# Performance work log

Measured on AMD Instinct MI355X. Metric: run time of the kernel, lower is better.

## Reference

```python
import jax, jax.numpy as jnp
import numpy as np

N_NODES = 100000


def _gcn_conv(x, W, b, src, dst, n):
    # PyG GCNConv (default): add self-loops, norm = deg^{-1/2}[src] * deg^{-1/2}[dst]
    # degree computed on target nodes (col) with unit edge weights, then
    # out[i] = sum_{(j->i)} norm_ji * (x_j @ W) + b
    loops = jnp.arange(n, dtype=src.dtype)
    s = jnp.concatenate([src, loops])
    d = jnp.concatenate([dst, loops])
    deg = jax.ops.segment_sum(jnp.ones_like(d, dtype=x.dtype), d, num_segments=n)
    dinv = jnp.where(deg > 0, jax.lax.rsqrt(deg), 0.0)
    h = x @ W                                  # [n, out_dim]
    norm = (dinv[s] * dinv[d])[:, None]        # [E+n, 1]
    msg = h[s] * norm                          # gather + scale
    out = jax.ops.segment_sum(msg, d, num_segments=n)  # scatter-add to targets
    return out + b


def setup_inputs() -> dict:
    key = jax.random.key(0)
    ks = jax.random.split(key, 4)
    x = jax.random.normal(ks[0], (N_NODES, 128), dtype=jnp.float32)
    edge_index = jax.random.randint(ks[1], (2, 1600000), 0, N_NODES, dtype=jnp.int64)
    W1 = jax.random.normal(ks[2], (128, 16), dtype=jnp.float32) * (1.0 / np.sqrt(128))
    b1 = jnp.zeros((16,), dtype=jnp.float32)
    W2 = jax.random.normal(ks[3], (16, 3), dtype=jnp.float32) * (1.0 / np.sqrt(16))
    b2 = jnp.zeros((3,), dtype=jnp.float32)
    return {"x": x, "edge_index": edge_index, "W1": W1, "b1": b1, "W2": W2, "b2": b2}


def reference(x, edge_index, W1, b1, W2, b2):
    src, dst = edge_index[0], edge_index[1]
    n = x.shape[0]
    h = _gcn_conv(x, W1, b1, src, dst, n)
    h = jax.nn.relu(h)
    # F.dropout in eval mode == identity (deterministic baseline)
    h = _gcn_conv(h, W2, b2, src, dst, n)
    return jax.nn.log_softmax(h, axis=1)
```

## Files before the change

### kernel.cpp

```cpp
#include <hip/hip_runtime.h>
#include <hip/hip_fp16.h>
#include <math.h>


#define BSH 9
#define BNODES 512
#define P1 512
#define GROWS 64
#define K2BUF 10240
#define BCAP 12288
#define EPT 16

struct alignas(8) Half4 { __half x, y, z, w; };

__global__ void k1a_count(const int* __restrict__ dst, int* __restrict__ hist_t,
                          int NBK, int E) {
    __shared__ int lh[256];
    int t = threadIdx.x;
    lh[t] = 0;
    __syncthreads();
    int slice = (E + P1 - 1) / P1;
    int e0 = blockIdx.x * slice, e1 = min(E, e0 + slice);
    for (int e = e0 + t; e < e1; e += 256)
        atomicAdd(&lh[dst[e] >> BSH], 1);
    __syncthreads();
    for (int i = t; i < NBK; i += 256)
        hist_t[(size_t)i * P1 + blockIdx.x] = lh[i];
}

__global__ void kscan1(const int* __restrict__ hist_t, int* __restrict__ colpre_t,
                       int* __restrict__ btot, int NBK) {
    __shared__ int v[P1], part[256];
    int kb = blockIdx.x, t = threadIdx.x;
    v[t] = hist_t[(size_t)kb * P1 + t];
    v[t + 256] = hist_t[(size_t)kb * P1 + t + 256];
    __syncthreads();
    int a = v[2 * t], c = v[2 * t + 1];
    part[t] = a + c;
    __syncthreads();
    for (int o = 1; o < 256; o <<= 1) {
        int add = (t >= o) ? part[t - o] : 0;
        __syncthreads();
        part[t] += add;
        __syncthreads();
    }
    int pre = (t == 0) ? 0 : part[t - 1];
    colpre_t[(size_t)kb * P1 + 2 * t] = pre;
    colpre_t[(size_t)kb * P1 + 2 * t + 1] = pre + a;
    if (t == 255) btot[kb] = part[255];
}

__global__ void k1b_fat(const int* __restrict__ src, const int* __restrict__ dst,
                        const int* __restrict__ colpre_t,
                        unsigned int* __restrict__ staging,
                        const float* __restrict__ x, const float* __restrict__ W1,
                        Half4* __restrict__ g1h, int NBK, int n, int E) {
    __shared__ float sx[GROWS * 132];
    __shared__ float4 sW4[512];
    int b = blockIdx.x;
    if (b < P1) {
        int* hist  = (int*)sx;
        int* cs    = hist + 256;
        int* loff  = hist + 512;
        int* cur   = hist + 768;
        int* buf   = hist + 1024;
        int* gaddr = buf + 3200;
        int t = threadIdx.x;
        hist[t] = 0; cur[t] = 0;
        for (int i = t; i < NBK; i += 256)
            loff[i] = i * BCAP + colpre_t[(size_t)i * P1 + b];
        __syncthreads();
        int slice = (E + P1 - 1) / P1;
        int e0 = b * slice, e1 = min(E, e0 + slice);
        int len = e1 - e0;
        int dl[EPT], sl[EPT];
        int cnt = 0;
        for (int e = e0 + t; e < e1 && cnt < EPT; e += 256, ++cnt) {
            dl[cnt] = dst[e];
            sl[cnt] = src[e];
        }
        for (int i = 0; i < cnt; ++i)
            atomicAdd(&hist[dl[i] >> BSH], 1);
        __syncthreads();
        int h = hist[t];
        cs[t] = h;
        __syncthreads();
        for (int o = 1; o < 256; o <<= 1) {
            int add = (t >= o) ? cs[t - o] : 0;
            __syncthreads();
            cs[t] += add;
            __syncthreads();
        }
        int incl = cs[t];
        __syncthreads();
        cs[t] = incl - h;
        __syncthreads();
        for (int i = 0; i < cnt; ++i) {
            int d = dl[i], s = sl[i];
            int k = d >> BSH;
            int tk = atomicAdd(&cur[k], 1);
            int pos = cs[k] + tk;
            buf[pos] = (s << BSH) | (d & (BNODES - 1));
            gaddr[pos] = loff[k] + tk;
        }
        __syncthreads();
        for (int p = t; p < len; p += 256)
            staging[gaddr[p]] = (unsigned int)buf[p];
    } else {
        int t = threadIdx.x;
        int base = (b - P1) * GROWS;
        for (int i = t; i < 512; i += 256) sW4[i] = ((const float4*)W1)[i];
        for (int i = t; i < GROWS * 32; i += 256) {
            int r = i >> 5, c = i & 31;
            int row = base + r;
            float4 v = (row < n) ? ((const float4*)x)[(size_t)row * 32 + c]
                                 : make_float4(0.f, 0.f, 0.f, 0.f);
            *((float4*)&sx[r * 132 + c * 4]) = v;
        }
        __syncthreads();
        int r = t >> 2, c4 = t & 3;
        int row = base + r;
        if (row >= n) return;
        float4 acc = make_float4(0.f, 0.f, 0.f, 0.f);
        #pragma unroll 8
        for (int q = 0; q < 32; ++q) {
            float4 xv = *((const float4*)&sx[r * 132 + q * 4]);
            #pragma unroll
            for (int j = 0; j < 4; ++j) {
                float s = (j == 0) ? xv.x : (j == 1) ? xv.y : (j == 2) ? xv.z : xv.w;
                float4 w = sW4[(q * 4 + j) * 4 + c4];
                acc.x += s * w.x; acc.y += s * w.y; acc.z += s * w.z; acc.w += s * w.w;
            }
        }
        Half4 hh;
        hh.x = __float2half(acc.x); hh.y = __float2half(acc.y);
        hh.z = __float2half(acc.z); hh.w = __float2half(acc.w);
        g1h[(size_t)row * 4 + c4] = hh;
    }
}

__global__ void __launch_bounds__(1024) k2_bucket(
        const unsigned int* __restrict__ staging, const int* __restrict__ btot,
        int* __restrict__ csr, int* __restrict__ deg, float* __restrict__ dinv,
        int* __restrict__ row_start, Half4* __restrict__ g1h, int n) {
    __shared__ int lh[BNODES], sc[BNODES], lcur[BNODES];
    __shared__ float ldv[BNODES];
    __shared__ int buf[K2BUF];
    int kb = blockIdx.x, t = threadIdx.x;
    int node0 = kb << BSH;
    int nloc = min(BNODES, n - node0);
    int ebase = kb * BCAP;
    int ecnt = btot[kb];
    if (t < BNODES) { lh[t] = 0; lcur[t] = 0; }
    __syncthreads();
    for (int e = t; e < ecnt; e += 1024)
        atomicAdd(&lh[staging[ebase + e] & (BNODES - 1)], 1);
    __syncthreads();
    int own = 0;
    if (t < BNODES) { own = lh[t]; sc[t] = own; }
    __syncthreads();
    for (int o = 1; o < BNODES; o <<= 1) {
        int add = 0;
        if (t < BNODES && t >= o) add = sc[t - o];
        __syncthreads();
        if (t < BNODES) sc[t] += add;
        __syncthreads();
    }
    if (t < BNODES) {
        int excl = sc[t] - own;
        if (t < nloc) {
            deg[node0 + t] = own;
            row_start[node0 + t] = ebase + excl;
            float dv = rsqrtf((float)(own + 1));
            dinv[node0 + t] = dv;
            ldv[t] = dv;
        }
        sc[t] = excl;
    }
    __syncthreads();
    if (ecnt <= K2BUF) {
        for (int e = t; e < ecnt; e += 1024) {
            unsigned int p = staging[ebase + e];
            int loc = p & (BNODES - 1);
            int tk = atomicAdd(&lcur[loc], 1);
            buf[sc[loc] + tk] = (int)(p >> BSH);
        }
        __syncthreads();
        for (int p = t; p < ecnt; p += 1024)
            csr[ebase + p] = buf[p];
    } else {
        for (int e = t; e < ecnt; e += 1024) {
            unsigned int p = staging[ebase + e];
            int loc = p & (BNODES - 1);
            int tk = atomicAdd(&lcur[loc], 1);
            csr[ebase + sc[loc] + tk] = (int)(p >> BSH);
        }
    }
    for (int j = t; j < nloc * 4; j += 1024) {
        float dv = ldv[j >> 2];
        Half4 v = g1h[(size_t)node0 * 4 + j];
        v.x = __float2half(__half2float(v.x) * dv);
        v.y = __float2half(__half2float(v.y) * dv);
        v.z = __float2half(__half2float(v.z) * dv);
        v.w = __float2half(__half2float(v.w) * dv);
        g1h[(size_t)node0 * 4 + j] = v;
    }
}

__global__ void k_gather1(const uint4* __restrict__ g1q, const int* __restrict__ csr,
                          const int* __restrict__ row_start, const int* __restrict__ deg,
                          const float* __restrict__ dinv, const float* __restrict__ b1,
                          const float* __restrict__ W2, Half4* __restrict__ g2h, int n) {
    int idx = blockIdx.x * 256 + threadIdx.x;
    int i = idx >> 4, l = idx & 15;
    if (i >= n) return;
    int off = row_start[i], dg = deg[i];
    float acc[16];
    #pragma unroll
    for (int j = 0; j < 16; ++j) acc[j] = 0.f;
    if (l == 0) {
        uint4 p0 = g1q[2 * (size_t)i], p1 = g1q[2 * (size_t)i + 1];
        const __half2* h0 = reinterpret_cast<const __half2*>(&p0);
        const __half2* h1 = reinterpret_cast<const __half2*>(&p1);
        #pragma unroll
        for (int j = 0; j < 4; ++j) {
            float2 f0 = __half22float2(h0[j]);
            float2 f1 = __half22float2(h1[j]);
            acc[2 * j] += f0.x; acc[2 * j + 1] += f0.y;
            acc[8 + 2 * j] += f1.x; acc[9 + 2 * j] += f1.y;
        }
    }
    for (int k = l; k < dg; k += 16) {
        int s = csr[off + k];
        uint4 p0 = g1q[2 * (size_t)s], p1 = g1q[2 * (size_t)s + 1];
        const __half2* h0 = reinterpret_cast<const __half2*>(&p0);
        const __half2* h1 = reinterpret_cast<const __half2*>(&p1);
        #pragma unroll
        for (int j = 0; j < 4; ++j) {
            float2 f0 = __half22float2(h0[j]);
            float2 f1 = __half22float2(h1[j]);
            acc[2 * j] += f0.x; acc[2 * j + 1] += f0.y;
            acc[8 + 2 * j] += f1.x; acc[9 + 2 * j] += f1.y;
        }
    }
    #pragma unroll
    for (int j = 0; j < 8; ++j) {
        float send = (l & 1) ? acc[j] : acc[j + 8];
        float recv = __shfl_xor(send, 1);
        acc[j] = ((l & 1) ? acc[j + 8] : acc[j]) + recv;
    }
    #pragma unroll
    for (int j = 0; j < 4; ++j) {
        float send = (l & 2) ? acc[j] : acc[j + 4];
        float recv = __shfl_xor(send, 2);
        acc[j] = ((l & 2) ? acc[j + 4] : acc[j]) + recv;
    }
    #pragma unroll
    for (int j = 0; j < 2; ++j) {
        float send = (l & 4) ? acc[j] : acc[j + 2];
        float recv = __shfl_xor(send, 4);
        acc[j] = ((l & 4) ? acc[j + 2] : acc[j]) + recv;
    }
    {
        float send = (l & 8) ? acc[0] : acc[1];
        float recv = __shfl_xor(send, 8);
        acc[0] = ((l & 8) ? acc[1] : acc[0]) + recv;
    }
    int f = ((l & 1) << 3) | ((l & 2) << 1) | ((l & 4) >> 1) | ((l & 8) >> 3);
    float di = dinv[i];
    float z = fmaxf(0.f, di * acc[0] + b1[f]);
    float o0 = z * W2[f * 3 + 0];
    float o1 = z * W2[f * 3 + 1];
    float o2 = z * W2[f * 3 + 2];
    #pragma unroll
    for (int m = 1; m < 16; m <<= 1) {
        o0 += __shfl_xor(o0, m);
        o1 += __shfl_xor(o1, m);
        o2 += __shfl_xor(o2, m);
    }
    if (l != 0) return;
    Half4 g;
    g.x = __float2half(di * o0); g.y = __float2half(di * o1);
    g.z = __float2half(di * o2); g.w = __float2half(0.f);
    g2h[i] = g;
}

__global__ void k_gather2(const Half4* __restrict__ g2h, const int* __restrict__ csr,
                          const int* __restrict__ row_start, const int* __restrict__ deg,
                          const float* __restrict__ dinv, const float* __restrict__ b2,
                          float* __restrict__ out, int n) {
    int idx = blockIdx.x * 256 + threadIdx.x;
    int i = idx >> 4, l = idx & 15;
    if (i >= n) return;
    int off = row_start[i], dg = deg[i];
    float v0 = 0.f, v1 = 0.f, v2 = 0.f;
    if (l == 0) {
        Half4 s = g2h[i];
        v0 = __half2float(s.x); v1 = __half2float(s.y); v2 = __half2float(s.z);
    }
    for (int e = l; e < dg; e += 16) {
        int s = csr[off + e];
        Half4 g = g2h[s];
        v0 += __half2float(g.x); v1 += __half2float(g.y); v2 += __half2float(g.z);
    }
    #pragma unroll
    for (int o = 1; o < 16; o <<= 1) {
        v0 += __shfl_xor(v0, o);
        v1 += __shfl_xor(v1, o);
        v2 += __shfl_xor(v2, o);
    }
    if (l >= 3) return;
    float di = dinv[i];
    float a0 = di * v0 + b2[0];
    float a1 = di * v1 + b2[1];
    float a2 = di * v2 + b2[2];
    float m = fmaxf(a0, fmaxf(a1, a2));
    float lse = logf(expf(a0 - m) + expf(a1 - m) + expf(a2 - m));
    float r = (l == 0) ? a0 : (l == 1) ? a1 : a2;
    out[(size_t)i * 3 + l] = r - m - lse;
}

extern "C" void kernel_launch(void* const* d_in, const int* in_sizes, int n_in,
                              void* d_out, int out_size, void* d_ws, size_t ws_size,
                              hipStream_t stream) {
    const float* x  = (const float*)d_in[0];
    const int*   ei = (const int*)d_in[1];
    const float* W1 = (const float*)d_in[2];
    const float* b1 = (const float*)d_in[3];
    const float* W2 = (const float*)d_in[4];
    const float* b2 = (const float*)d_in[5];
    float* out = (float*)d_out;

    const int n = in_sizes[0] / 128;
    const int E = in_sizes[1] / 2;
    const int* src = ei;
    const int* dst = ei + E;

    const int NBK = (n + BNODES - 1) >> BSH;

    auto align = [](size_t v) { return (v + 255) & ~(size_t)255; };
    char* ws = (char*)d_ws;
    size_t o = 0;
    int* hist_t   = (int*)(ws + o); o = align(o + (size_t)NBK * P1 * 4);
    int* colpre_t = (int*)(ws + o); o = align(o + (size_t)NBK * P1 * 4);
    int* btot     = (int*)(ws + o); o = align(o + (size_t)NBK * 4);
    int* deg      = (int*)(ws + o); o = align(o + (size_t)n * 4);
    float* dinv   = (float*)(ws + o); o = align(o + (size_t)n * 4);
    int* row_start= (int*)(ws + o); o = align(o + (size_t)n * 4);
    unsigned int* staging = (unsigned int*)(ws + o); o = align(o + (size_t)NBK * BCAP * 4);
    int* csr      = (int*)(ws + o); o = align(o + (size_t)NBK * BCAP * 4);
    Half4* g1h    = (Half4*)(ws + o); o = align(o + (size_t)n * 4 * 8);
    Half4* g2h    = (Half4*)(ws + o); o = align(o + (size_t)n * 8);

    const int B = 256;
    int gGemm = (n + GROWS - 1) / GROWS;
    int gn16  = (16 * n + B - 1) / B;

    k1a_count<<<P1, B, 0, stream>>>(dst, hist_t, NBK, E);
    kscan1<<<NBK, B, 0, stream>>>(hist_t, colpre_t, btot, NBK);
    k1b_fat<<<P1 + gGemm, B, 0, stream>>>(src, dst, colpre_t, staging,
                                          x, W1, g1h, NBK, n, E);
    k2_bucket<<<NBK, 1024, 0, stream>>>(staging, btot, csr, deg, dinv, row_start, g1h, n);
    k_gather1<<<gn16, B, 0, stream>>>((const uint4*)g1h, csr, row_start, deg, dinv, b1, W2,
                                      g2h, n);
    k_gather2<<<gn16, B, 0, stream>>>(g2h, csr, row_start, deg, dinv, b2, out, n);
}
```

Measured before the change: 164.6 us.

## Replace count+scan prepass with global atomic bucket cursors in bucketing kernel

Removes the separate histogram-count and column-scan kernels. Each partition block now reserves its slice of every destination bucket with one global atomicAdd on a padded per-bucket cursor, which is zeroed by a memset. This cuts two launches and a full pass over dst, at the cost of nondeterministic edge order within buckets and dropping edges past the bucket capacity. k2_bucket also keeps its staged entries in registers so it reads staging once instead of twice.

```diff
diff --git a/kernel.cpp b/kernel.cpp
--- a/kernel.cpp
+++ b/kernel.cpp
@@ -10,48 +10,13 @@
 #define K2BUF 10240
 #define BCAP 12288
 #define EPT 16
+#define EPT2 12
+#define CSTR 16
 
 struct alignas(8) Half4 { __half x, y, z, w; };
 
-__global__ void k1a_count(const int* __restrict__ dst, int* __restrict__ hist_t,
-                          int NBK, int E) {
-    __shared__ int lh[256];
-    int t = threadIdx.x;
-    lh[t] = 0;
-    __syncthreads();
-    int slice = (E + P1 - 1) / P1;
-    int e0 = blockIdx.x * slice, e1 = min(E, e0 + slice);
-    for (int e = e0 + t; e < e1; e += 256)
-        atomicAdd(&lh[dst[e] >> BSH], 1);
-    __syncthreads();
-    for (int i = t; i < NBK; i += 256)
-        hist_t[(size_t)i * P1 + blockIdx.x] = lh[i];
-}
-
-__global__ void kscan1(const int* __restrict__ hist_t, int* __restrict__ colpre_t,
-                       int* __restrict__ btot, int NBK) {
-    __shared__ int v[P1], part[256];
-    int kb = blockIdx.x, t = threadIdx.x;
-    v[t] = hist_t[(size_t)kb * P1 + t];
-    v[t + 256] = hist_t[(size_t)kb * P1 + t + 256];
-    __syncthreads();
-    int a = v[2 * t], c = v[2 * t + 1];
-    part[t] = a + c;
-    __syncthreads();
-    for (int o = 1; o < 256; o <<= 1) {
-        int add = (t >= o) ? part[t - o] : 0;
-        __syncthreads();
-        part[t] += add;
-        __syncthreads();
-    }
-    int pre = (t == 0) ? 0 : part[t - 1];
-    colpre_t[(size_t)kb * P1 + 2 * t] = pre;
-    colpre_t[(size_t)kb * P1 + 2 * t + 1] = pre + a;
-    if (t == 255) btot[kb] = part[255];
-}
-
 __global__ void k1b_fat(const int* __restrict__ src, const int* __restrict__ dst,
-                        const int* __restrict__ colpre_t,
+                        int* __restrict__ cursor,
                         unsigned int* __restrict__ staging,
                         const float* __restrict__ x, const float* __restrict__ W1,
                         Half4* __restrict__ g1h, int NBK, int n, int E) {
@@ -61,14 +26,12 @@
     if (b < P1) {
         int* hist  = (int*)sx;
         int* cs    = hist + 256;
-        int* loff  = hist + 512;
+        int* rbase = hist + 512;
         int* cur   = hist + 768;
         int* buf   = hist + 1024;
         int* gaddr = buf + 3200;
         int t = threadIdx.x;
         hist[t] = 0; cur[t] = 0;
-        for (int i = t; i < NBK; i += 256)
-            loff[i] = i * BCAP + colpre_t[(size_t)i * P1 + b];
         __syncthreads();
         int slice = (E + P1 - 1) / P1;
         int e0 = b * slice, e1 = min(E, e0 + slice);
@@ -94,6 +57,7 @@
         int incl = cs[t];
         __syncthreads();
         cs[t] = incl - h;
+        rbase[t] = (h > 0 && t < NBK) ? atomicAdd(&cursor[t * CSTR], h) : 0;
         __syncthreads();
         for (int i = 0; i < cnt; ++i) {
             int d = dl[i], s = sl[i];
@@ -101,11 +65,14 @@
             int tk = atomicAdd(&cur[k], 1);
             int pos = cs[k] + tk;
             buf[pos] = (s << BSH) | (d & (BNODES - 1));
-            gaddr[pos] = loff[k] + tk;
-        }
-        __syncthreads();
-        for (int p = t; p < len; p += 256)
-            staging[gaddr[p]] = (unsigned int)buf[p];
+            int g = rbase[k] + tk;
+            gaddr[pos] = (g < BCAP) ? (k * BCAP + g) : -1;
+        }
+        __syncthreads();
+        for (int p = t; p < len; p += 256) {
+            int a = gaddr[p];
+            if (a >= 0) staging[a] = (unsigned int)buf[p];
+        }
     } else {
         int t = threadIdx.x;
         int base = (b - P1) * GROWS;
@@ -140,7 +107,7 @@
 }
 
 __global__ void __launch_bounds__(1024) k2_bucket(
-        const unsigned int* __restrict__ staging, const int* __restrict__ btot,
+        const unsigned int* __restrict__ staging, const int* __restrict__ cursor,
         int* __restrict__ csr, int* __restrict__ deg, float* __restrict__ dinv,
         int* __restrict__ row_start, Half4* __restrict__ g1h, int n) {
     __shared__ int lh[BNODES], sc[BNODES], lcur[BNODES];
@@ -150,11 +117,15 @@
     int node0 = kb << BSH;
     int nloc = min(BNODES, n - node0);
     int ebase = kb * BCAP;
-    int ecnt = btot[kb];
+    int ecnt = min(cursor[kb * CSTR], BCAP);
     if (t < BNODES) { lh[t] = 0; lcur[t] = 0; }
     __syncthreads();
-    for (int e = t; e < ecnt; e += 1024)
-        atomicAdd(&lh[staging[ebase + e] & (BNODES - 1)], 1);
+    int el[EPT2];
+    int cnt = 0;
+    for (int e = t; e < ecnt && cnt < EPT2; e += 1024, ++cnt)
+        el[cnt] = (int)staging[ebase + e];
+    for (int i = 0; i < cnt; ++i)
+        atomicAdd(&lh[el[i] & (BNODES - 1)], 1);
     __syncthreads();
     int own = 0;
     if (t < BNODES) { own = lh[t]; sc[t] = own; }
@@ -179,21 +150,21 @@
     }
     __syncthreads();
     if (ecnt <= K2BUF) {
-        for (int e = t; e < ecnt; e += 1024) {
-            unsigned int p = staging[ebase + e];
+        for (int i = 0; i < cnt; ++i) {
+            int p = el[i];
             int loc = p & (BNODES - 1);
             int tk = atomicAdd(&lcur[loc], 1);
-            buf[sc[loc] + tk] = (int)(p >> BSH);
+            buf[sc[loc] + tk] = p >> BSH;
         }
         __syncthreads();
         for (int p = t; p < ecnt; p += 1024)
             csr[ebase + p] = buf[p];
     } else {
-        for (int e = t; e < ecnt; e += 1024) {
-            unsigned int p = staging[ebase + e];
+        for (int i = 0; i < cnt; ++i) {
+            int p = el[i];
             int loc = p & (BNODES - 1);
             int tk = atomicAdd(&lcur[loc], 1);
-            csr[ebase + sc[loc] + tk] = (int)(p >> BSH);
+            csr[ebase + sc[loc] + tk] = p >> BSH;
         }
     }
     for (int j = t; j < nloc * 4; j += 1024) {
@@ -341,9 +312,7 @@
     auto align = [](size_t v) { return (v + 255) & ~(size_t)255; };
     char* ws = (char*)d_ws;
     size_t o = 0;
-    int* hist_t   = (int*)(ws + o); o = align(o + (size_t)NBK * P1 * 4);
-    int* colpre_t = (int*)(ws + o); o = align(o + (size_t)NBK * P1 * 4);
-    int* btot     = (int*)(ws + o); o = align(o + (size_t)NBK * 4);
+    int* cursor   = (int*)(ws + o); o = align(o + (size_t)NBK * CSTR * 4);
     int* deg      = (int*)(ws + o); o = align(o + (size_t)n * 4);
     float* dinv   = (float*)(ws + o); o = align(o + (size_t)n * 4);
     int* row_start= (int*)(ws + o); o = align(o + (size_t)n * 4);
@@ -356,11 +325,10 @@
     int gGemm = (n + GROWS - 1) / GROWS;
     int gn16  = (16 * n + B - 1) / B;
 
-    k1a_count<<<P1, B, 0, stream>>>(dst, hist_t, NBK, E);
-    kscan1<<<NBK, B, 0, stream>>>(hist_t, colpre_t, btot, NBK);
-    k1b_fat<<<P1 + gGemm, B, 0, stream>>>(src, dst, colpre_t, staging,
+    hipMemsetAsync(cursor, 0, (size_t)NBK * CSTR * 4, stream);
+    k1b_fat<<<P1 + gGemm, B, 0, stream>>>(src, dst, cursor, staging,
                                           x, W1, g1h, NBK, n, E);
-    k2_bucket<<<NBK, 1024, 0, stream>>>(staging, btot, csr, deg, dinv, row_start, g1h, n);
+    k2_bucket<<<NBK, 1024, 0, stream>>>(staging, cursor, csr, deg, dinv, row_start, g1h, n);
     k_gather1<<<gn16, B, 0, stream>>>((const uint4*)g1h, csr, row_start, deg, dinv, b1, W2,
                                       g2h, n);
     k_gather2<<<gn16, B, 0, stream>>>(g2h, csr, row_start, deg, dinv, b2, out, n);
```

Result: no change. 166.8 us (+1.3%).
